# Kernel tuning notes

Measured on AMD Instinct MI355X. Metric: run time of the kernel, lower is better.

## Reference

```python
import jax, jax.numpy as jnp
import numpy as np

HEADS = 8
HID = 256
D = HID // HEADS
NEG_SLOPE = 0.2  # PyG leaky_relu negative_slope default in HANConv
NA, NPAP, CIN = 10000, 20000, 256
E = 256000
OUT = 16


def seg_softmax(scores, seg, num_segments):
    # scores: [E, H]; softmax over edges sharing the same dst segment id
    m = jax.ops.segment_max(scores, seg, num_segments=num_segments)
    m = jnp.where(jnp.isfinite(m), m, 0.0)
    e = jnp.exp(scores - m[seg])
    s = jax.ops.segment_sum(e, seg, num_segments=num_segments)
    return e / (s[seg] + 1e-16)


def han_edge(h_src, h_dst, att_src, att_dst, src, dst, num_dst):
    # h_src: [Ns, H, D]; att_*: [H, D]; src/dst: [E]
    a = (h_src * att_src).sum(-1)[src] + (h_dst * att_dst).sum(-1)[dst]  # [E, H]
    alpha = seg_softmax(jax.nn.leaky_relu(a, NEG_SLOPE), dst, num_dst)
    out = jax.ops.segment_sum(h_src[src] * alpha[..., None], dst, num_segments=num_dst)
    return jax.nn.relu(out.reshape(num_dst, HID))


def semantic_group(xs, q, k_W, k_b):
    out = jnp.stack(xs)                                            # [M, N, F]
    score = (jnp.tanh(out @ k_W + k_b) * q).sum(-1).mean(axis=1)   # [M]
    attn = jax.nn.softmax(score)                                   # softmax over metapaths
    return (out * attn[:, None, None]).sum(0)                      # [N, F]


def setup_inputs() -> dict:
    key = jax.random.key(0)
    ks = jax.random.split(key, 32)
    n = lambda i, shape, s: jax.random.normal(ks[i], shape, dtype=jnp.float32) * s
    ri = lambda i, hi: jax.random.randint(ks[i], (E,), 0, hi).astype(jnp.int64)
    w_scale = (1.0 / CIN) ** 0.5
    return {
        "x_author": n(0, (NA, CIN), 1.0),
        "x_paper": n(1, (NPAP, CIN), 1.0),
        "W_author": n(2, (CIN, HID), w_scale),
        "b_author": jnp.zeros((HID,), jnp.float32),
        "W_paper": n(3, (CIN, HID), w_scale),
        "b_paper": jnp.zeros((HID,), jnp.float32),
        "att_sw": n(4, (HEADS, D), 0.1),
        "att_dw": n(5, (HEADS, D), 0.1),
        "att_sc": n(6, (HEADS, D), 0.1),
        "att_dc": n(7, (HEADS, D), 0.1),
        "att_sr": n(8, (HEADS, D), 0.1),
        "att_dr": n(9, (HEADS, D), 0.1),
        "k_W": n(10, (HID, HID), (1.0 / HID) ** 0.5),
        "k_b": jnp.zeros((HID,), jnp.float32),
        "q": n(11, (HID,), 0.1),
        "lin_W": n(12, (HID, OUT), (1.0 / HID) ** 0.5),
        "lin_b": jnp.zeros((OUT,), jnp.float32),
        "ew_src": ri(13, NA), "ew_dst": ri(14, NPAP),
        "ec_src": ri(15, NPAP), "ec_dst": ri(16, NPAP),
        "er_src": ri(17, NPAP), "er_dst": ri(18, NA),
    }


def reference(x_author, x_paper, W_author, b_author, W_paper, b_paper,
              att_sw, att_dw, att_sc, att_dc, att_sr, att_dr,
              k_W, k_b, q, lin_W, lin_b,
              ew_src, ew_dst, ec_src, ec_dst, er_src, er_dst):
    # per-node-type projection -> [N, H, D]
    h_a = (x_author @ W_author + b_author).reshape(NA, HEADS, D)
    h_p = (x_paper @ W_paper + b_paper).reshape(NPAP, HEADS, D)
    # per-edge-type gather / attention / segment-softmax / scatter
    o_writes = han_edge(h_a, h_p, att_sw, att_dw, ew_src, ew_dst, NPAP)  # author->paper
    o_cites = han_edge(h_p, h_p, att_sc, att_dc, ec_src, ec_dst, NPAP)   # paper->paper
    o_rev = han_edge(h_p, h_a, att_sr, att_dr, er_src, er_dst, NA)       # paper->author
    # semantic-level attention over metapaths per dst node type
    paper_out = semantic_group([o_writes, o_cites], q, k_W, k_b)
    author_out = semantic_group([o_rev], q, k_W, k_b)
    # global_add_pool per node type (batch=None -> single graph) + shared linear
    pooled = jnp.stack([author_out.sum(0), paper_out.sum(0)])  # [2, HID]
    return pooled @ lin_W + lin_b                              # [2, OUT]
```

## Files before the change

kernel.cpp:

```cpp
#include <hip/hip_runtime.h>
#include <hip/hip_bf16.h>

#define HEADS 8
#define HID 256
#define NA 10000
#define NPAP 20000
#define NE 256000
#define N_SEG (2 * NPAP + NA)
#define TOTE (3 * NE)
#define NEG_SLOPE 0.2f
#define NBA 157
#define NBP 313
#define PROJ_BLKS (NBA + NBP)
#define DEG_BLKS 3000
#define NATT_BLKS (NPAP + NA)
#define NBS ((N_SEG + 255) / 256)
#define SCORE_BLKS (2 * NBP)
#define COLSUM_BLKS ((N_SEG + 31) / 32)

typedef __attribute__((ext_vector_type(8))) short bf16x8;
typedef __attribute__((ext_vector_type(4))) float f32x4;

__device__ __forceinline__ short f2bf(float x) {
    unsigned u = __float_as_uint(x);
    unsigned r = (u + 0x7fffu + ((u >> 16) & 1u)) >> 16;
    return (short)r;
}
__device__ __forceinline__ float bf2f(short s) {
    return __uint_as_float(((unsigned)(unsigned short)s) << 16);
}

__global__ __launch_bounds__(256) void wconv(
    const float* __restrict__ W_a, short* __restrict__ WaT,
    const float* __restrict__ W_p, short* __restrict__ WpT,
    const float* __restrict__ k_W, short* __restrict__ kWT)
{
    __shared__ short T[64][65];
    int b = blockIdx.x;
    int t = threadIdx.x;
    int z = b >> 4, rem = b & 15;
    int k0 = (rem & 3) * 64, c0 = (rem >> 2) * 64;
    const float* W = z == 0 ? W_a : (z == 1 ? W_p : k_W);
    short* Wt      = z == 0 ? WaT : (z == 1 ? WpT : kWT);
    int rr = t >> 6, c = t & 63;
#pragma unroll
    for (int p = 0; p < 16; ++p) {
        int r = rr + p * 4;
        T[c][r] = f2bf(W[(size_t)(k0 + r) * 256 + c0 + c]);
    }
    __syncthreads();
#pragma unroll
    for (int p = 0; p < 16; ++p) {
        int cc = rr + p * 4;
        Wt[(size_t)(c0 + cc) * 256 + k0 + c] = T[cc][c];
    }
}

__global__ __launch_bounds__(256) void proj_deg(
    const float* __restrict__ A0, const short* __restrict__ Wt0, const float* __restrict__ b0,
    short* __restrict__ C0, unsigned char* __restrict__ H80,
    const float* __restrict__ A1, const short* __restrict__ Wt1, const float* __restrict__ b1,
    short* __restrict__ C1, unsigned char* __restrict__ H81,
    const int* __restrict__ ewd, const int* __restrict__ ecd, const int* __restrict__ erd,
    int* __restrict__ deg4, unsigned short* __restrict__ rank16)
{
    __shared__ short As[64][64];
    __shared__ short Ws[256][64];

    int b = blockIdx.x;
    int t = threadIdx.x;

    if (b >= PROJ_BLKS) {
        int bb = b - PROJ_BLKS;
        int e = bb * 256 + t;
        if (e >= TOTE) return;
        int d;
        if (e < NE)          d = ewd[e];
        else if (e < 2 * NE) d = ecd[e - NE] + NPAP;
        else                 d = erd[e - 2 * NE] + 2 * NPAP;
        int r = atomicAdd(&deg4[(bb & 3) * N_SEG + d], 1);
        rank16[e] = (unsigned short)r;
        return;
    }

    const float* A; const short* Wt; const float* bias; short* Cb; unsigned char* H8; int N, row0;
    if (b < NBA) { A = A0; Wt = Wt0; bias = b0; Cb = C0; H8 = H80; N = NA;   row0 = b * 64; }
    else         { A = A1; Wt = Wt1; bias = b1; Cb = C1; H8 = H81; N = NPAP; row0 = (b - NBA) * 64; }

    int w = t >> 6, l = t & 63;
    int lr = l & 15, lh = l >> 4;
    int swz = (l & 7) << 3;

    f32x4 acc[4][4] = {};

    for (int k0 = 0; k0 < 256; k0 += 64) {
#pragma unroll
        for (int i = 0; i < 4; ++i) {
            int lin = t + i * 256;
            int r = lin >> 4, fc = (lin & 15) << 2;
            float4 v = make_float4(0.f, 0.f, 0.f, 0.f);
            int gr = row0 + r;
            if (gr < N) v = *reinterpret_cast<const float4*>(&A[(size_t)gr * 256 + k0 + fc]);
            short4 o;
            o.x = f2bf(v.x); o.y = f2bf(v.y); o.z = f2bf(v.z); o.w = f2bf(v.w);
            *reinterpret_cast<short4*>(&As[r][fc ^ ((r & 7) << 3)]) = o;
        }
#pragma unroll
        for (int i = 0; i < 8; ++i) {
            int lin = t + i * 256;
            int c = lin >> 3, kc = (lin & 7) << 3;
            *reinterpret_cast<bf16x8*>(&Ws[c][kc ^ ((c & 7) << 3)]) =
                *reinterpret_cast<const bf16x8*>(&Wt[(size_t)c * 256 + k0 + kc]);
        }
        __syncthreads();
#pragma unroll
        for (int kk = 0; kk < 64; kk += 32) {
            int krow = (kk + lh * 8) ^ swz;
            bf16x8 af[4], bfr[4];
#pragma unroll
            for (int mi = 0; mi < 4; ++mi)
                af[mi] = *reinterpret_cast<bf16x8*>(&As[mi * 16 + lr][krow]);
#pragma unroll
            for (int ni = 0; ni < 4; ++ni)
                bfr[ni] = *reinterpret_cast<bf16x8*>(&Ws[w * 64 + ni * 16 + lr][krow]);
#pragma unroll
            for (int mi = 0; mi < 4; ++mi)
#pragma unroll
                for (int ni = 0; ni < 4; ++ni)
                    acc[mi][ni] = __builtin_amdgcn_mfma_f32_16x16x32_bf16(
                        af[mi], bfr[ni], acc[mi][ni], 0, 0, 0);
        }
        __syncthreads();
    }

#pragma unroll
    for (int mi = 0; mi < 4; ++mi) {
        int rb = row0 + mi * 16 + lh * 4;
#pragma unroll
        for (int ni = 0; ni < 4; ++ni) {
            int c = w * 64 + ni * 16 + lr;
            float bc = bias[c];
#pragma unroll
            for (int j = 0; j < 4; ++j) {
                if (rb + j < N) {
                    float v = acc[mi][ni][j] + bc;
                    Cb[(size_t)(rb + j) * 256 + c] = f2bf(v);
                    unsigned pk = __builtin_amdgcn_cvt_pk_fp8_f32(v, v, 0, false);
                    H8[(size_t)(rb + j) * 256 + c] = (unsigned char)pk;
                }
            }
        }
    }
}

__global__ __launch_bounds__(256) void natt_scan(
    const short* __restrict__ h_p, const short* __restrict__ h_a,
    const float* __restrict__ att_dw, const float* __restrict__ att_sc,
    const float* __restrict__ att_dc, const float* __restrict__ att_sr,
    const float* __restrict__ att_sw, const float* __restrict__ att_dr,
    float* __restrict__ a_dw, float* __restrict__ a_sc,
    float* __restrict__ a_dc, float* __restrict__ a_sr,
    float* __restrict__ a_sw, float* __restrict__ a_dr,
    const int* __restrict__ deg4, int* __restrict__ excl, int* __restrict__ bsum)
{
    int b = blockIdx.x;
    int t = threadIdx.x;

    if (b >= NATT_BLKS) {
        __shared__ int buf[256];
        int bb = b - NATT_BLKS;
        int idx = bb * 256 + t;
        int v = 0;
        if (idx < N_SEG)
            v = deg4[idx] + deg4[N_SEG + idx] + deg4[2 * N_SEG + idx] + deg4[3 * N_SEG + idx];
        buf[t] = v;
        __syncthreads();
        for (int off = 1; off < 256; off <<= 1) {
            int add = (t >= off) ? buf[t - off] : 0;
            __syncthreads();
            buf[t] += add;
            __syncthreads();
        }
        if (idx < N_SEG) excl[idx] = buf[t] - v;
        if (t == 255) bsum[bb] = buf[255];
        return;
    }

    if (b < NPAP) {
        float v = bf2f(h_p[(size_t)b * 256 + t]);
        float d0 = v * att_dw[t], d1 = v * att_sc[t], d2 = v * att_dc[t], d3 = v * att_sr[t];
#pragma unroll
        for (int k = 16; k > 0; k >>= 1) {
            d0 += __shfl_xor(d0, k, 64);
            d1 += __shfl_xor(d1, k, 64);
            d2 += __shfl_xor(d2, k, 64);
            d3 += __shfl_xor(d3, k, 64);
        }
        if ((t & 31) == 0) {
            int hh = t >> 5;
            a_dw[b * 8 + hh] = d0; a_sc[b * 8 + hh] = d1;
            a_dc[b * 8 + hh] = d2; a_sr[b * 8 + hh] = d3;
        }
    } else {
        int m = b - NPAP;
        float v = bf2f(h_a[(size_t)m * 256 + t]);
        float d0 = v * att_sw[t], d1 = v * att_dr[t];
#pragma unroll
        for (int k = 16; k > 0; k >>= 1) {
            d0 += __shfl_xor(d0, k, 64);
            d1 += __shfl_xor(d1, k, 64);
        }
        if ((t & 31) == 0) {
            int hh = t >> 5;
            a_sw[m * 8 + hh] = d0; a_dr[m * 8 + hh] = d1;
        }
    }
}

__global__ void scan_l2(const int* __restrict__ bsum, int* __restrict__ boff, int nb)
{
    __shared__ int buf[256];
    int t = threadIdx.x;
    int v = (t < nb) ? bsum[t] : 0;
    buf[t] = v;
    __syncthreads();
    for (int off = 1; off < 256; off <<= 1) {
        int add = (t >= off) ? buf[t - off] : 0;
        __syncthreads();
        buf[t] += add;
        __syncthreads();
    }
    if (t < nb) boff[t] = buf[t] - v;
}

__global__ void scan_l3(const int* __restrict__ excl, const int* __restrict__ boff,
                        const int* __restrict__ deg4,
                        int* __restrict__ starts, int* __restrict__ base4, int N)
{
    int i = blockIdx.x * 256 + threadIdx.x;
    if (i > N) return;
    int v = (i == N) ? TOTE : excl[i] + boff[i >> 8];
    starts[i] = v;
    if (i < N) {
        int c = v;
        base4[i] = c;                 c += deg4[i];
        base4[N_SEG + i] = c;         c += deg4[N_SEG + i];
        base4[2 * N_SEG + i] = c;     c += deg4[2 * N_SEG + i];
        base4[3 * N_SEG + i] = c;
    }
}

__global__ __launch_bounds__(256) void scatter_edges(
    const int* __restrict__ ews, const int* __restrict__ ewd,
    const int* __restrict__ ecs, const int* __restrict__ ecd,
    const int* __restrict__ ers, const int* __restrict__ erd,
    const int* __restrict__ base4, const unsigned short* __restrict__ rank16,
    int* __restrict__ ssrc)
{
    int e = blockIdx.x * 256 + threadIdx.x;
    if (e >= TOTE) return;
    int s, d;
    if (e < NE)          { s = ews[e];          d = ewd[e]; }
    else if (e < 2 * NE) { s = ecs[e - NE];     d = ecd[e - NE] + NPAP; }
    else                 { s = ers[e - 2 * NE]; d = erd[e - 2 * NE] + 2 * NPAP; }
    int shadow = (e >> 8) & 3;
    int pos = base4[shadow * N_SEG + d] + (int)rank16[e];
    ssrc[pos] = s;
}

__global__ __launch_bounds__(256) void han_seg(
    const int* __restrict__ starts, const int* __restrict__ ssrc,
    const float* __restrict__ a_sw, const float* __restrict__ a_dw,
    const float* __restrict__ a_sc, const float* __restrict__ a_dc,
    const float* __restrict__ a_sr, const float* __restrict__ a_dr,
    const unsigned* __restrict__ h8_a, const unsigned* __restrict__ h8_p,
    short* __restrict__ outall)
{
    int w = threadIdx.x >> 6, lane = threadIdx.x & 63;
    int n = blockIdx.x * 4 + w;
    if (n >= N_SEG) return;

    const float* asrc; const float* adst; const unsigned* h8;
    int nloc;
    if (n < NPAP)          { nloc = n;            asrc = a_sw; adst = a_dw; h8 = h8_a; }
    else if (n < 2 * NPAP) { nloc = n - NPAP;     asrc = a_sc; adst = a_dc; h8 = h8_p; }
    else                   { nloc = n - 2 * NPAP; asrc = a_sr; adst = a_dr; h8 = h8_p; }

    int hh = lane >> 3;
    int c0 = lane << 2;
    float ad = adst[nloc * 8 + hh];

    int i = starts[n], end = starts[n + 1];
    float ac0 = 0.f, ac1 = 0.f, ac2 = 0.f, ac3 = 0.f, ps = 0.f;

    for (; i + 4 <= end; i += 4) {
        int s0 = __builtin_amdgcn_readfirstlane(ssrc[i]);
        int s1 = __builtin_amdgcn_readfirstlane(ssrc[i + 1]);
        int s2 = __builtin_amdgcn_readfirstlane(ssrc[i + 2]);
        int s3 = __builtin_amdgcn_readfirstlane(ssrc[i + 3]);
        float x0 = asrc[s0 * 8 + hh] + ad;
        float x1 = asrc[s1 * 8 + hh] + ad;
        float x2 = asrc[s2 * 8 + hh] + ad;
        float x3 = asrc[s3 * 8 + hh] + ad;
        unsigned v0 = h8[s0 * 64 + lane];
        unsigned v1 = h8[s1 * 64 + lane];
        unsigned v2 = h8[s2 * 64 + lane];
        unsigned v3 = h8[s3 * 64 + lane];
        x0 = x0 > 0.f ? x0 : NEG_SLOPE * x0;
        x1 = x1 > 0.f ? x1 : NEG_SLOPE * x1;
        x2 = x2 > 0.f ? x2 : NEG_SLOPE * x2;
        x3 = x3 > 0.f ? x3 : NEG_SLOPE * x3;
        float e0 = __expf(x0), e1 = __expf(x1), e2 = __expf(x2), e3 = __expf(x3);
        ps += (e0 + e1) + (e2 + e3);
        ac0 += e0 * __builtin_amdgcn_cvt_f32_fp8(v0, 0) + e1 * __builtin_amdgcn_cvt_f32_fp8(v1, 0)
             + e2 * __builtin_amdgcn_cvt_f32_fp8(v2, 0) + e3 * __builtin_amdgcn_cvt_f32_fp8(v3, 0);
        ac1 += e0 * __builtin_amdgcn_cvt_f32_fp8(v0, 1) + e1 * __builtin_amdgcn_cvt_f32_fp8(v1, 1)
             + e2 * __builtin_amdgcn_cvt_f32_fp8(v2, 1) + e3 * __builtin_amdgcn_cvt_f32_fp8(v3, 1);
        ac2 += e0 * __builtin_amdgcn_cvt_f32_fp8(v0, 2) + e1 * __builtin_amdgcn_cvt_f32_fp8(v1, 2)
             + e2 * __builtin_amdgcn_cvt_f32_fp8(v2, 2) + e3 * __builtin_amdgcn_cvt_f32_fp8(v3, 2);
        ac3 += e0 * __builtin_amdgcn_cvt_f32_fp8(v0, 3) + e1 * __builtin_amdgcn_cvt_f32_fp8(v1, 3)
             + e2 * __builtin_amdgcn_cvt_f32_fp8(v2, 3) + e3 * __builtin_amdgcn_cvt_f32_fp8(v3, 3);
    }
    for (; i < end; ++i) {
        int s0 = __builtin_amdgcn_readfirstlane(ssrc[i]);
        float x0 = asrc[s0 * 8 + hh] + ad;
        unsigned v0 = h8[s0 * 64 + lane];
        x0 = x0 > 0.f ? x0 : NEG_SLOPE * x0;
        float e0 = __expf(x0);
        ps += e0;
        ac0 += e0 * __builtin_amdgcn_cvt_f32_fp8(v0, 0);
        ac1 += e0 * __builtin_amdgcn_cvt_f32_fp8(v0, 1);
        ac2 += e0 * __builtin_amdgcn_cvt_f32_fp8(v0, 2);
        ac3 += e0 * __builtin_amdgcn_cvt_f32_fp8(v0, 3);
    }

    float inv = 1.0f / (ps + 1e-16f);
    float o0 = ac0 * inv, o1 = ac1 * inv, o2 = ac2 * inv, o3 = ac3 * inv;
    short4 o;
    o.x = f2bf(o0 > 0.f ? o0 : 0.f);
    o.y = f2bf(o1 > 0.f ? o1 : 0.f);
    o.z = f2bf(o2 > 0.f ? o2 : 0.f);
    o.w = f2bf(o3 > 0.f ? o3 : 0.f);
    *reinterpret_cast<short4*>(&outall[(size_t)n * 256 + c0]) = o;
}

__global__ __launch_bounds__(256) void score_colsum(
    const short* __restrict__ outall, const short* __restrict__ Wt,
    const float* __restrict__ kb, const float* __restrict__ q,
    float* __restrict__ score, float* __restrict__ cw, float* __restrict__ cc,
    float* __restrict__ cr)
{
    __shared__ short As[64][64];
    __shared__ short Ws[256][64];
    __shared__ float red[256];

    int b = blockIdx.x;
    int t = threadIdx.x;

    if (b >= SCORE_BLKS) {
        int r0 = (b - SCORE_BLKS) * 32;
        int rend = r0 + 32 < N_SEG ? r0 + 32 : N_SEG;
        float s = 0.f;
        for (int r = r0; r < rend; ++r) s += bf2f(outall[(size_t)r * 256 + t]);
        float* cs = r0 < NPAP ? cw : (r0 < 2 * NPAP ? cc : cr);
        atomicAdd(&cs[t], s);
        return;
    }

    const short* A; float* sAcc; int row0;
    if (b < NBP) { A = outall;                           sAcc = score + 0; row0 = b * 64; }
    else         { A = outall + (size_t)NPAP * HID;      sAcc = score + 1; row0 = (b - NBP) * 64; }
    const int N = NPAP;

    int w = t >> 6, l = t & 63;
    int lr = l & 15, lh = l >> 4;
    int swz = (l & 7) << 3;

    f32x4 acc[4][4] = {};

    for (int k0 = 0; k0 < 256; k0 += 64) {
#pragma unroll
        for (int i = 0; i < 2; ++i) {
            int lin = t + i * 256;
            int r = lin >> 3, kc = (lin & 7) << 3;
            bf16x8 v = {};
            int gr = row0 + r;
            if (gr < N) v = *reinterpret_cast<const bf16x8*>(&A[(size_t)gr * 256 + k0 + kc]);
            *reinterpret_cast<bf16x8*>(&As[r][kc ^ ((r & 7) << 3)]) = v;
        }
#pragma unroll
        for (int i = 0; i < 8; ++i) {
            int lin = t + i * 256;
            int c = lin >> 3, kc = (lin & 7) << 3;
            *reinterpret_cast<bf16x8*>(&Ws[c][kc ^ ((c & 7) << 3)]) =
                *reinterpret_cast<const bf16x8*>(&Wt[(size_t)c * 256 + k0 + kc]);
        }
        __syncthreads();
#pragma unroll
        for (int kk = 0; kk < 64; kk += 32) {
            int krow = (kk + lh * 8) ^ swz;
            bf16x8 af[4], bfr[4];
#pragma unroll
            for (int mi = 0; mi < 4; ++mi)
                af[mi] = *reinterpret_cast<bf16x8*>(&As[mi * 16 + lr][krow]);
#pragma unroll
            for (int ni = 0; ni < 4; ++ni)
                bfr[ni] = *reinterpret_cast<bf16x8*>(&Ws[w * 64 + ni * 16 + lr][krow]);
#pragma unroll
            for (int mi = 0; mi < 4; ++mi)
#pragma unroll
                for (int ni = 0; ni < 4; ++ni)
                    acc[mi][ni] = __builtin_amdgcn_mfma_f32_16x16x32_bf16(
                        af[mi], bfr[ni], acc[mi][ni], 0, 0, 0);
        }
        __syncthreads();
    }

    float s = 0.f;
#pragma unroll
    for (int mi = 0; mi < 4; ++mi) {
        int rb = row0 + mi * 16 + lh * 4;
#pragma unroll
        for (int ni = 0; ni < 4; ++ni) {
            int c = w * 64 + ni * 16 + lr;
            float bc = kb[c], qc = q[c];
#pragma unroll
            for (int j = 0; j < 4; ++j) {
                if (rb + j < N) s += tanhf(acc[mi][ni][j] + bc) * qc;
            }
        }
    }
    red[t] = s;
    __syncthreads();
    for (int k = 128; k > 0; k >>= 1) {
        if (t < k) red[t] += red[t + k];
        __syncthreads();
    }
    if (t == 0) atomicAdd(sAcc, red[0]);
}

__global__ void finalize(const float* __restrict__ scoreAcc,
                         const float* __restrict__ colsum_w, const float* __restrict__ colsum_c,
                         const float* __restrict__ colsum_r,
                         const float* __restrict__ lin_W, const float* __restrict__ lin_b,
                         float* __restrict__ out)
{
    int t = threadIdx.x;
    if (t >= 32) return;
    float sw = scoreAcc[0] / (float)NPAP;
    float scs = scoreAcc[1] / (float)NPAP;
    float mx = fmaxf(sw, scs);
    float ew = expf(sw - mx), ec = expf(scs - mx);
    float aw = ew / (ew + ec), ac = ec / (ew + ec);
    int row = t >> 4, j = t & 15;
    float acc = lin_b[j];
    for (int c = 0; c < 256; ++c) {
        float p = (row == 0) ? colsum_r[c] : (aw * colsum_w[c] + ac * colsum_c[c]);
        acc += p * lin_W[c * 16 + j];
    }
    out[row * 16 + j] = acc;
}

extern "C" void kernel_launch(void* const* d_in, const int* in_sizes, int n_in,
                              void* d_out, int out_size, void* d_ws, size_t ws_size,
                              hipStream_t stream)
{
    const float* x_a   = (const float*)d_in[0];
    const float* x_p   = (const float*)d_in[1];
    const float* W_a   = (const float*)d_in[2];
    const float* b_a   = (const float*)d_in[3];
    const float* W_p   = (const float*)d_in[4];
    const float* b_p   = (const float*)d_in[5];
    const float* att_sw = (const float*)d_in[6];
    const float* att_dw = (const float*)d_in[7];
    const float* att_sc = (const float*)d_in[8];
    const float* att_dc = (const float*)d_in[9];
    const float* att_sr = (const float*)d_in[10];
    const float* att_dr = (const float*)d_in[11];
    const float* k_W   = (const float*)d_in[12];
    const float* k_b   = (const float*)d_in[13];
    const float* q     = (const float*)d_in[14];
    const float* lin_W = (const float*)d_in[15];
    const float* lin_b = (const float*)d_in[16];
    const int* ew_src = (const int*)d_in[17];
    const int* ew_dst = (const int*)d_in[18];
    const int* ec_src = (const int*)d_in[19];
    const int* ec_dst = (const int*)d_in[20];
    const int* er_src = (const int*)d_in[21];
    const int* er_dst = (const int*)d_in[22];

    float* ws = (float*)d_ws;
    size_t off = 0;
    auto align4 = [&]() { off = (off + 3) & ~(size_t)3; };

    short* h_a_bf = (short*)(ws + off); off += (size_t)NA * HID / 2;
    short* h_p_bf = (short*)(ws + off); off += (size_t)NPAP * HID / 2;
    unsigned char* h8_a = (unsigned char*)(ws + off); off += (size_t)NA * HID / 4;
    unsigned char* h8_p = (unsigned char*)(ws + off); off += (size_t)NPAP * HID / 4;
    short* WaT  = (short*)(ws + off); off += 256 * 256 / 2;
    short* WpT  = (short*)(ws + off); off += 256 * 256 / 2;
    short* kWT  = (short*)(ws + off); off += 256 * 256 / 2;
    float* a_sw = ws + off; off += (size_t)NA * 8;
    float* a_dw = ws + off; off += (size_t)NPAP * 8;
    float* a_sc = ws + off; off += (size_t)NPAP * 8;
    float* a_dc = ws + off; off += (size_t)NPAP * 8;
    float* a_sr = ws + off; off += (size_t)NPAP * 8;
    float* a_dr = ws + off; off += (size_t)NA * 8;
    short* outall = (short*)(ws + off); off += (size_t)N_SEG * HID / 2;
    int* starts  = (int*)(ws + off); off += N_SEG + 1; align4();
    int* base4   = (int*)(ws + off); off += 4 * N_SEG; align4();
    int* sexcl   = (int*)(ws + off); off += N_SEG + 1; align4();
    int* sbsum   = (int*)(ws + off); off += 256;
    int* sboff   = (int*)(ws + off); off += 256;
    int* ssrc    = (int*)(ws + off); off += TOTE;
    unsigned short* rank16 = (unsigned short*)(ws + off); off += TOTE / 2;
    size_t zero_start = off;
    int* deg4       = (int*)(ws + off); off += 4 * N_SEG; align4();
    float* colsum_w = ws + off; off += 256;
    float* colsum_c = ws + off; off += 256;
    float* colsum_r = ws + off; off += 256;
    float* score    = ws + off; off += 2;
    size_t zero_bytes = (off - zero_start) * sizeof(float);

    hipMemsetAsync(ws + zero_start, 0, zero_bytes, stream);

    wconv<<<48, 256, 0, stream>>>(W_a, WaT, W_p, WpT, k_W, kWT);

    proj_deg<<<PROJ_BLKS + DEG_BLKS, 256, 0, stream>>>(
        x_a, WaT, b_a, h_a_bf, h8_a,
        x_p, WpT, b_p, h_p_bf, h8_p,
        ew_dst, ec_dst, er_dst, deg4, rank16);

    natt_scan<<<NATT_BLKS + NBS, 256, 0, stream>>>(
        h_p_bf, h_a_bf, att_dw, att_sc, att_dc, att_sr, att_sw, att_dr,
        a_dw, a_sc, a_dc, a_sr, a_sw, a_dr,
        deg4, sexcl, sbsum);

    scan_l2<<<1, 256, 0, stream>>>(sbsum, sboff, NBS);
    scan_l3<<<(N_SEG + 1 + 255) / 256, 256, 0, stream>>>(sexcl, sboff, deg4, starts, base4, N_SEG);

    scatter_edges<<<(TOTE + 255) / 256, 256, 0, stream>>>(ew_src, ew_dst, ec_src, ec_dst,
                                                          er_src, er_dst, base4, rank16, ssrc);

    han_seg<<<(N_SEG + 3) / 4, 256, 0, stream>>>(starts, ssrc, a_sw, a_dw, a_sc, a_dc, a_sr, a_dr,
                                                 (const unsigned*)h8_a, (const unsigned*)h8_p,
                                                 outall);

    score_colsum<<<SCORE_BLKS + COLSUM_BLKS, 256, 0, stream>>>(
        outall, kWT, k_b, q, score, colsum_w, colsum_c, colsum_r);

    finalize<<<1, 64, 0, stream>>>(score, colsum_w, colsum_c, colsum_r, lin_W, lin_b, (float*)d_out);
}
```

Baseline: 233.6 us.

## Split projection GEMM into column tiles and separate colsum from score GEMM

The projection GEMM now tiles 64 output columns per block, giving four times as many blocks, each with a smaller LDS footprint (64x64 weights instead of 256x64) and fewer accumulators. This is meant to raise occupancy and improve load balance across CUs. The trade-off is that each A tile is reloaded and converted from fp32 four times. The fused score/colsum kernel is also split into two launches, which removes the mixed-role branching but adds a kernel launch.

```diff
diff --git a/kernel.cpp b/kernel.cpp
--- a/kernel.cpp
+++ b/kernel.cpp
@@ -11,12 +11,10 @@
 #define NEG_SLOPE 0.2f
 #define NBA 157
 #define NBP 313
-#define PROJ_BLKS (NBA + NBP)
+#define PROJ_BLKS (4 * (NBA + NBP))
 #define DEG_BLKS 3000
 #define NATT_BLKS (NPAP + NA)
 #define NBS ((N_SEG + 255) / 256)
-#define SCORE_BLKS (2 * NBP)
-#define COLSUM_BLKS ((N_SEG + 31) / 32)
 
 typedef __attribute__((ext_vector_type(8))) short bf16x8;
 typedef __attribute__((ext_vector_type(4))) float f32x4;
@@ -65,7 +63,7 @@
     int* __restrict__ deg4, unsigned short* __restrict__ rank16)
 {
     __shared__ short As[64][64];
-    __shared__ short Ws[256][64];
+    __shared__ short Ws2[64][64];
 
     int b = blockIdx.x;
     int t = threadIdx.x;
@@ -83,15 +81,18 @@
         return;
     }
 
-    const float* A; const short* Wt; const float* bias; short* Cb; unsigned char* H8; int N, row0;
-    if (b < NBA) { A = A0; Wt = Wt0; bias = b0; Cb = C0; H8 = H80; N = NA;   row0 = b * 64; }
-    else         { A = A1; Wt = Wt1; bias = b1; Cb = C1; H8 = H81; N = NPAP; row0 = (b - NBA) * 64; }
+    const float* A; const short* Wt; const float* bias; short* Cb; unsigned char* H8; int N, row0, col0;
+    if (b < 4 * NBA) { A = A0; Wt = Wt0; bias = b0; Cb = C0; H8 = H80; N = NA;
+                       row0 = (b >> 2) * 64; col0 = (b & 3) * 64; }
+    else             { int bb = b - 4 * NBA;
+                       A = A1; Wt = Wt1; bias = b1; Cb = C1; H8 = H81; N = NPAP;
+                       row0 = (bb >> 2) * 64; col0 = (bb & 3) * 64; }
 
     int w = t >> 6, l = t & 63;
     int lr = l & 15, lh = l >> 4;
     int swz = (l & 7) << 3;
 
-    f32x4 acc[4][4] = {};
+    f32x4 acc[4] = {};
 
     for (int k0 = 0; k0 < 256; k0 += 64) {
 #pragma unroll
@@ -106,48 +107,40 @@
             *reinterpret_cast<short4*>(&As[r][fc ^ ((r & 7) << 3)]) = o;
         }
 #pragma unroll
-        for (int i = 0; i < 8; ++i) {
+        for (int i = 0; i < 2; ++i) {
             int lin = t + i * 256;
             int c = lin >> 3, kc = (lin & 7) << 3;
-            *reinterpret_cast<bf16x8*>(&Ws[c][kc ^ ((c & 7) << 3)]) =
-                *reinterpret_cast<const bf16x8*>(&Wt[(size_t)c * 256 + k0 + kc]);
+            *reinterpret_cast<bf16x8*>(&Ws2[c][kc ^ ((c & 7) << 3)]) =
+                *reinterpret_cast<const bf16x8*>(&Wt[(size_t)(col0 + c) * 256 + k0 + kc]);
         }
         __syncthreads();
 #pragma unroll
         for (int kk = 0; kk < 64; kk += 32) {
             int krow = (kk + lh * 8) ^ swz;
-            bf16x8 af[4], bfr[4];
-#pragma unroll
-            for (int mi = 0; mi < 4; ++mi)
-                af[mi] = *reinterpret_cast<bf16x8*>(&As[mi * 16 + lr][krow]);
+            bf16x8 af = *reinterpret_cast<bf16x8*>(&As[w * 16 + lr][krow]);
+            bf16x8 bfr[4];
 #pragma unroll
             for (int ni = 0; ni < 4; ++ni)
-                bfr[ni] = *reinterpret_cast<bf16x8*>(&Ws[w * 64 + ni * 16 + lr][krow]);
-#pragma unroll
-            for (int mi = 0; mi < 4; ++mi)
-#pragma unroll
-                for (int ni = 0; ni < 4; ++ni)
-                    acc[mi][ni] = __builtin_amdgcn_mfma_f32_16x16x32_bf16(
-                        af[mi], bfr[ni], acc[mi][ni], 0, 0, 0);
-        }
-        __syncthreads();
-    }
-
-#pragma unroll
-    for (int mi = 0; mi < 4; ++mi) {
-        int rb = row0 + mi * 16 + lh * 4;
-#pragma unroll
-        for (int ni = 0; ni < 4; ++ni) {
-            int c = w * 64 + ni * 16 + lr;
-            float bc = bias[c];
-#pragma unroll
-            for (int j = 0; j < 4; ++j) {
-                if (rb + j < N) {
-                    float v = acc[mi][ni][j] + bc;
-                    Cb[(size_t)(rb + j) * 256 + c] = f2bf(v);
-                    unsigned pk = __builtin_amdgcn_cvt_pk_fp8_f32(v, v, 0, false);
-                    H8[(size_t)(rb + j) * 256 + c] = (unsigned char)pk;
-                }
+                bfr[ni] = *reinterpret_cast<bf16x8*>(&Ws2[ni * 16 + lr][krow]);
+#pragma unroll
+            for (int ni = 0; ni < 4; ++ni)
+                acc[ni] = __builtin_amdgcn_mfma_f32_16x16x32_bf16(af, bfr[ni], acc[ni], 0, 0, 0);
+        }
+        __syncthreads();
+    }
+
+    int rb = row0 + w * 16 + lh * 4;
+#pragma unroll
+    for (int ni = 0; ni < 4; ++ni) {
+        int c = col0 + ni * 16 + lr;
+        float bc = bias[c];
+#pragma unroll
+        for (int j = 0; j < 4; ++j) {
+            if (rb + j < N) {
+                float v = acc[ni][j] + bc;
+                Cb[(size_t)(rb + j) * 256 + c] = f2bf(v);
+                unsigned pk = __builtin_amdgcn_cvt_pk_fp8_f32(v, v, 0, false);
+                H8[(size_t)(rb + j) * 256 + c] = (unsigned char)pk;
             }
         }
     }
@@ -344,35 +337,36 @@
     *reinterpret_cast<short4*>(&outall[(size_t)n * 256 + c0]) = o;
 }
 
-__global__ __launch_bounds__(256) void score_colsum(
-    const short* __restrict__ outall, const short* __restrict__ Wt,
-    const float* __restrict__ kb, const float* __restrict__ q,
-    float* __restrict__ score, float* __restrict__ cw, float* __restrict__ cc,
-    float* __restrict__ cr)
+__global__ void colsum3(const short* __restrict__ outall,
+                        float* __restrict__ cw, float* __restrict__ cc,
+                        float* __restrict__ cr)
+{
+    int t = threadIdx.x;
+    int r0 = blockIdx.x * 32;
+    int rend = r0 + 32 < N_SEG ? r0 + 32 : N_SEG;
+    float s = 0.f;
+    for (int r = r0; r < rend; ++r) s += bf2f(outall[(size_t)r * 256 + t]);
+    float* cs = r0 < NPAP ? cw : (r0 < 2 * NPAP ? cc : cr);
+    atomicAdd(&cs[t], s);
+}
+
+__global__ __launch_bounds__(256) void gemm_score(
+    const short* __restrict__ A0, const short* __restrict__ Wt, const float* __restrict__ kb,
+    float* __restrict__ sAcc0, int N0, int nb0,
+    const short* __restrict__ A1, float* __restrict__ sAcc1, int N1,
+    const float* __restrict__ q)
 {
     __shared__ short As[64][64];
     __shared__ short Ws[256][64];
     __shared__ float red[256];
 
-    int b = blockIdx.x;
-    int t = threadIdx.x;
-
-    if (b >= SCORE_BLKS) {
-        int r0 = (b - SCORE_BLKS) * 32;
-        int rend = r0 + 32 < N_SEG ? r0 + 32 : N_SEG;
-        float s = 0.f;
-        for (int r = r0; r < rend; ++r) s += bf2f(outall[(size_t)r * 256 + t]);
-        float* cs = r0 < NPAP ? cw : (r0 < 2 * NPAP ? cc : cr);
-        atomicAdd(&cs[t], s);
-        return;
-    }
-
-    const short* A; float* sAcc; int row0;
-    if (b < NBP) { A = outall;                           sAcc = score + 0; row0 = b * 64; }
-    else         { A = outall + (size_t)NPAP * HID;      sAcc = score + 1; row0 = (b - NBP) * 64; }
-    const int N = NPAP;
-
-    int w = t >> 6, l = t & 63;
+    int bx = blockIdx.x;
+    const short* A; float* sAcc; int N, row0;
+    if (bx < nb0) { A = A0; sAcc = sAcc0; N = N0; row0 = bx * 64; }
+    else          { A = A1; sAcc = sAcc1; N = N1; row0 = (bx - nb0) * 64; }
+
+    int tid = threadIdx.x;
+    int w = tid >> 6, l = tid & 63;
     int lr = l & 15, lh = l >> 4;
     int swz = (l & 7) << 3;
 
@@ -381,7 +375,7 @@
     for (int k0 = 0; k0 < 256; k0 += 64) {
 #pragma unroll
         for (int i = 0; i < 2; ++i) {
-            int lin = t + i * 256;
+            int lin = tid + i * 256;
             int r = lin >> 3, kc = (lin & 7) << 3;
             bf16x8 v = {};
             int gr = row0 + r;
@@ -390,7 +384,7 @@
         }
 #pragma unroll
         for (int i = 0; i < 8; ++i) {
-            int lin = t + i * 256;
+            int lin = tid + i * 256;
             int c = lin >> 3, kc = (lin & 7) << 3;
             *reinterpret_cast<bf16x8*>(&Ws[c][kc ^ ((c & 7) << 3)]) =
                 *reinterpret_cast<const bf16x8*>(&Wt[(size_t)c * 256 + k0 + kc]);
@@ -430,13 +424,13 @@
             }
         }
     }
-    red[t] = s;
+    red[tid] = s;
     __syncthreads();
     for (int k = 128; k > 0; k >>= 1) {
-        if (t < k) red[t] += red[t + k];
-        __syncthreads();
-    }
-    if (t == 0) atomicAdd(sAcc, red[0]);
+        if (tid < k) red[tid] += red[tid + k];
+        __syncthreads();
+    }
+    if (tid == 0) atomicAdd(sAcc, red[0]);
 }
 
 __global__ void finalize(const float* __restrict__ scoreAcc,
@@ -546,8 +540,10 @@
                                                  (const unsigned*)h8_a, (const unsigned*)h8_p,
                                                  outall);
 
-    score_colsum<<<SCORE_BLKS + COLSUM_BLKS, 256, 0, stream>>>(
-        outall, kWT, k_b, q, score, colsum_w, colsum_c, colsum_r);
+    colsum3<<<(N_SEG + 31) / 32, 256, 0, stream>>>(outall, colsum_w, colsum_c, colsum_r);
+    gemm_score<<<2 * NBP, 256, 0, stream>>>(
+        outall, kWT, k_b, score + 0, NPAP, NBP,
+        outall + (size_t)NPAP * HID, score + 1, NPAP, q);
 
     finalize<<<1, 64, 0, stream>>>(score, colsum_w, colsum_c, colsum_r, lin_W, lin_b, (float*)d_out);
 }
```

Result: slower. 245.8 us (+5.2%).
